# Kernel tuning notes

Hardware: AMD Instinct MI355X
Metric: run time of the kernel (lower is better)

The kernel has to match this reference:

```python
import jax, jax.numpy as jnp
import numpy as np

L_LEVELS = 16
N_FEATS = 2
BASE_RES = 16
LOG2_T = 19
T = 2 ** LOG2_T
BOUND = 1.0
DESIRED_RES = 2048 * BOUND
PER_LEVEL_SCALE = np.exp2(np.log2(DESIRED_RES / BASE_RES) / (L_LEVELS - 1))
PRIMES = np.array([1, 2654435761, 805459861], dtype=np.uint32)
# 8 trilinear corner offsets, [8,3]
OFFSETS = np.array([[(i >> d) & 1 for d in range(3)] for i in range(8)], dtype=np.uint32)


def hash_encode(x, table):
    """x: [N,3] in [-bound,bound]; table: [L, T, F]. Returns [N, L*F]."""
    x01 = jnp.clip((x + BOUND) / (2.0 * BOUND), 0.0, 1.0)  # [N,3]
    feats = []
    for l in range(L_LEVELS):
        scale = BASE_RES * (PER_LEVEL_SCALE ** l) - 1.0  # torch-ngp gridencoder convention
        res = int(np.ceil(scale)) + 1
        pos = x01 * jnp.float32(scale) + 0.5
        pg = jnp.floor(pos)
        frac = pos - pg                                   # [N,3]
        pgi = pg.astype(jnp.uint32)
        corners = pgi[:, None, :] + OFFSETS[None, :, :]   # [N,8,3] uint32
        if res ** 3 <= T:
            # grid small enough: direct (strided) indexing
            r = np.uint32(res)
            idx = corners[..., 0] + corners[..., 1] * r + corners[..., 2] * (r * r)
        else:
            # spatial hash (xor of coord*prime)
            idx = (corners[..., 0] * PRIMES[0]) ^ (corners[..., 1] * PRIMES[1]) ^ (corners[..., 2] * PRIMES[2])
        idx = (idx % np.uint32(T)).astype(jnp.int32)      # [N,8]
        f = table[l][idx]                                 # [N,8,F] gather
        # trilinear weights: prod over dims of frac (if corner bit=1) else 1-frac
        w = jnp.prod(jnp.where(OFFSETS[None, :, :] == 1, frac[:, None, :], 1.0 - frac[:, None, :]), axis=-1)  # [N,8]
        feats.append(jnp.sum(f * w[..., None], axis=1))   # [N,F]
    return jnp.concatenate(feats, axis=-1)                # [N, L*F]


def softplus_beta100(x):
    z = 100.0 * x
    return jnp.where(z > 20.0, x, jnp.log1p(jnp.exp(jnp.minimum(z, 20.0))) / 100.0)


def setup_inputs() -> dict:
    key = jax.random.key(0)
    k = jax.random.split(key, 6)
    N = 1048576
    in_dim = L_LEVELS * N_FEATS  # 32
    hidden = 64
    out_dim = 1 + 15             # sdf + geo_feat
    x = jax.random.uniform(k[0], (N, 3), jnp.float32, -1.0, 1.0)
    table = jax.random.uniform(k[1], (L_LEVELS, T, N_FEATS), jnp.float32, -1e-4, 1e-4)
    W0 = jax.random.normal(k[2], (hidden, in_dim), jnp.float32) * (1.0 / np.sqrt(in_dim))
    b0 = jnp.zeros((hidden,), jnp.float32)
    W1 = jax.random.normal(k[3], (out_dim, hidden), jnp.float32) * (1.0 / np.sqrt(hidden))
    b1 = jnp.zeros((out_dim,), jnp.float32)
    return {"x": x, "table": table, "W0": W0, "b0": b0, "W1": W1, "b1": b1}


def reference(x, table, W0, b0, W1, b1):
    enc = hash_encode(x, table)                      # [N,32]
    h = softplus_beta100(enc @ W0.T + b0)            # [N,64]
    h = h @ W1.T + b1                                # [N,16]
    sdf = h[..., :1]
    geo_feat = h[..., 1:]
    return (sdf, geo_feat)
```

## Files before the change

kernel.cpp:

```cpp
#include <hip/hip_runtime.h>
#include <math.h>

constexpr int      kLevels = 16;
constexpr unsigned kT      = 1u << 19;
constexpr int      kHidden = 64;
constexpr int      kInDim  = 32;
constexpr int      kOutDim = 16;

struct LevelParams {
    float    scale[kLevels];
    unsigned res[kLevels];
    unsigned dense[kLevels];
};

typedef __attribute__((ext_vector_type(8))) short bf16x8;
typedef __attribute__((ext_vector_type(4))) float f32x4;
typedef __attribute__((ext_vector_type(2))) unsigned uint2v;

__device__ inline float bf2f(unsigned short b) {
    unsigned u = ((unsigned)b) << 16;
    return __builtin_bit_cast(float, u);
}
__device__ inline unsigned short f2bf(float f) {
    unsigned u = __builtin_bit_cast(unsigned, f);
    unsigned r = (u + 0x7fffu + ((u >> 16) & 1u)) >> 16;
    return (unsigned short)r;
}
__device__ inline unsigned pack2bf(float a, float b) {
    return (unsigned)f2bf(a) | ((unsigned)f2bf(b) << 16);
}

__global__ __launch_bounds__(256) void convert_table(
        const float* __restrict__ t, unsigned* __restrict__ o, int n4)
{
    int i = blockIdx.x * blockDim.x + threadIdx.x;
    if (i >= n4) return;
    float4 v = ((const float4*)t)[i];
    ((uint2*)o)[i] = make_uint2(pack2bf(v.x, v.y), pack2bf(v.z, v.w));
}

__global__ __launch_bounds__(256) void encode_level(
        const float* __restrict__ x,
        const unsigned* __restrict__ tblAll,
        unsigned* __restrict__ enc,
        int N, LevelParams lp)
{
    const int l   = blockIdx.y;
    const int tid = threadIdx.x;
    const int pA  = blockIdx.x * 512 + tid;

    const float    scale = lp.scale[l];
    const unsigned res   = lp.res[l];
    const bool     dense = (lp.dense[l] != 0);
    const unsigned* tbl  = tblAll + (size_t)l * kT;

    #pragma unroll
    for (int half = 0; half < 2; ++half) {
        const int p = pA + half * 256;
        if (p >= N) continue;

        const float x0 = fminf(fmaxf((x[3 * p + 0] + 1.0f) * 0.5f, 0.0f), 1.0f);
        const float y0 = fminf(fmaxf((x[3 * p + 1] + 1.0f) * 0.5f, 0.0f), 1.0f);
        const float z0 = fminf(fmaxf((x[3 * p + 2] + 1.0f) * 0.5f, 0.0f), 1.0f);

        const float posx = x0 * scale + 0.5f;
        const float posy = y0 * scale + 0.5f;
        const float posz = z0 * scale + 0.5f;
        const float fgx = floorf(posx), fgy = floorf(posy), fgz = floorf(posz);
        const float fx = posx - fgx, fy = posy - fgy, fz = posz - fgz;
        const float gx = 1.0f - fx,  gy = 1.0f - fy,  gz = 1.0f - fz;
        const unsigned ix = (unsigned)fgx, iy = (unsigned)fgy, iz = (unsigned)fgz;

        unsigned v0[4], v1[4];
        float    wyz[4];

        #pragma unroll
        for (int c2 = 0; c2 < 4; ++c2) {
            const unsigned cy = iy + (c2 & 1);
            const unsigned cz = iz + (c2 >> 1);
            wyz[c2] = ((c2 & 1) ? fy : gy) * ((c2 >> 1) ? fz : gz);

            if (dense) {
                const unsigned base = cy * res + cz * res * res;
                const unsigned idx0 = (ix + base) & (kT - 1u);
                if ((idx0 & 1u) == 0u) {
                    const uint2v pr = *(const uint2v*)(tbl + idx0);
                    v0[c2] = pr.x; v1[c2] = pr.y;
                } else {
                    v0[c2] = tbl[idx0];
                    v1[c2] = tbl[idx0 + 1u];
                }
            } else {
                const unsigned base = (cy * 2654435761u) ^ (cz * 805459861u);
                const unsigned idx0 = (ix ^ base) & (kT - 1u);
                if ((ix & 1u) == 0u) {
                    const unsigned b = idx0 & ~1u;
                    const uint2v pr = *(const uint2v*)(tbl + b);
                    const bool sw = (idx0 & 1u) != 0u;
                    v0[c2] = sw ? pr.y : pr.x;
                    v1[c2] = sw ? pr.x : pr.y;
                } else {
                    const unsigned idx1 = ((ix + 1u) ^ base) & (kT - 1u);
                    v0[c2] = tbl[idx0];
                    v1[c2] = tbl[idx1];
                }
            }
        }

        float a0 = 0.0f, a1 = 0.0f;
        #pragma unroll
        for (int c2 = 0; c2 < 4; ++c2) {
            const float w0 = gx * wyz[c2];
            const float w1 = fx * wyz[c2];
            a0 = fmaf(bf2f((unsigned short)(v0[c2] & 0xffffu)), w0, a0);
            a1 = fmaf(bf2f((unsigned short)(v0[c2] >> 16)),     w0, a1);
            a0 = fmaf(bf2f((unsigned short)(v1[c2] & 0xffffu)), w1, a0);
            a1 = fmaf(bf2f((unsigned short)(v1[c2] >> 16)),     w1, a1);
        }
        enc[(size_t)l * N + p] = pack2bf(a0, a1);
    }
}

__global__ __launch_bounds__(256) void mlp_mfma(
        const unsigned* __restrict__ enc,
        const float* __restrict__ W0,
        const float* __restrict__ b0,
        const float* __restrict__ W1,
        const float* __restrict__ b1,
        float* __restrict__ out, int N, int nTiles)
{
    constexpr int kHStride = 72;
    __shared__ short lds_h[4][16 * kHStride];

    const int wave = threadIdx.x >> 6;
    const int lane = threadIdx.x & 63;
    const int quad = lane >> 4;
    const int l16  = lane & 15;

    union Frag { bf16x8 v; short s[8]; unsigned u[4]; };

    Frag w0f[4];
    #pragma unroll
    for (int hb = 0; hb < 4; ++hb) {
        #pragma unroll
        for (int j = 0; j < 8; ++j) {
            const int k = quad * 8 + j;
            const int n = hb * 16 + l16;
            w0f[hb].s[j] = (short)f2bf(W0[n * kInDim + k]);
        }
    }
    Frag w1f[2];
    #pragma unroll
    for (int kb = 0; kb < 2; ++kb) {
        #pragma unroll
        for (int j = 0; j < 8; ++j) {
            const int k = kb * 32 + quad * 8 + j;
            const int n = l16;
            w1f[kb].s[j] = (short)f2bf(W1[n * kHidden + k]);
        }
    }
    float b0v[4];
    #pragma unroll
    for (int hb = 0; hb < 4; ++hb) b0v[hb] = b0[hb * 16 + l16];
    const float b1v = b1[l16];

    short* hrow = lds_h[wave];
    const int waveGlobal = blockIdx.x * 4 + wave;
    const int nWaves     = gridDim.x * 4;

    for (int t = waveGlobal; t < nTiles; t += nWaves) {
        const int P = t * 16;
        int p = P + l16;
        if (p >= N) p = N - 1;

        Frag af;
        #pragma unroll
        for (int j2 = 0; j2 < 4; ++j2)
            af.u[j2] = enc[(size_t)(quad * 4 + j2) * N + p];

        f32x4 acc[4];
        #pragma unroll
        for (int hb = 0; hb < 4; ++hb) {
            acc[hb] = f32x4{b0v[hb], b0v[hb], b0v[hb], b0v[hb]};
            acc[hb] = __builtin_amdgcn_mfma_f32_16x16x32_bf16(
                          af.v, w0f[hb].v, acc[hb], 0, 0, 0);
        }

        #pragma unroll
        for (int hb = 0; hb < 4; ++hb) {
            #pragma unroll
            for (int r = 0; r < 4; ++r) {
                const float a = acc[hb][r];
                const float z = 100.0f * a;
                const float h = (z > 20.0f) ? a
                              : (__logf(1.0f + __expf(z)) * 0.01f);
                const int row = quad * 4 + r;
                const int col = hb * 16 + l16;
                hrow[row * kHStride + col] = (short)f2bf(h);
            }
        }
        bf16x8 h0 = *(const bf16x8*)&hrow[l16 * kHStride + quad * 8];
        bf16x8 h1 = *(const bf16x8*)&hrow[l16 * kHStride + 32 + quad * 8];

        f32x4 acc2 = f32x4{b1v, b1v, b1v, b1v};
        acc2 = __builtin_amdgcn_mfma_f32_16x16x32_bf16(h0, w1f[0].v, acc2, 0, 0, 0);
        acc2 = __builtin_amdgcn_mfma_f32_16x16x32_bf16(h1, w1f[1].v, acc2, 0, 0, 0);

        #pragma unroll
        for (int r = 0; r < 4; ++r) {
            const int pp = P + quad * 4 + r;
            if (pp < N) {
                if (l16 == 0) out[pp] = acc2[r];
                else out[(size_t)N + (size_t)pp * 15u + (l16 - 1)] = acc2[r];
            }
        }
    }
}

__global__ __launch_bounds__(256) void sdf_fused(
        const float* __restrict__ x, const float* __restrict__ table,
        const float* __restrict__ W0, const float* __restrict__ b0,
        const float* __restrict__ W1, const float* __restrict__ b1,
        float* __restrict__ out, int N, LevelParams lp)
{
    const int gid = blockIdx.x * blockDim.x + threadIdx.x;
    if (gid >= N) return;
    const float x0 = fminf(fmaxf((x[3 * gid + 0] + 1.0f) * 0.5f, 0.0f), 1.0f);
    const float y0 = fminf(fmaxf((x[3 * gid + 1] + 1.0f) * 0.5f, 0.0f), 1.0f);
    const float z0 = fminf(fmaxf((x[3 * gid + 2] + 1.0f) * 0.5f, 0.0f), 1.0f);
    float enc[kInDim];
    #pragma unroll
    for (int l = 0; l < kLevels; ++l) {
        const float scale = lp.scale[l];
        const unsigned res = lp.res[l];
        const bool dense = (lp.dense[l] != 0);
        const float posx = x0 * scale + 0.5f, posy = y0 * scale + 0.5f, posz = z0 * scale + 0.5f;
        const float fgx = floorf(posx), fgy = floorf(posy), fgz = floorf(posz);
        const float fx = posx - fgx, fy = posy - fgy, fz = posz - fgz;
        const float gx = 1.0f - fx, gy = 1.0f - fy, gz = 1.0f - fz;
        const unsigned ix = (unsigned)fgx, iy = (unsigned)fgy, iz = (unsigned)fgz;
        const float* tbl = table + (size_t)l * kT * 2u;
        float a0 = 0.0f, a1 = 0.0f;
        #pragma unroll
        for (int c = 0; c < 8; ++c) {
            const unsigned cx = ix + (c & 1), cy = iy + ((c >> 1) & 1), cz = iz + ((c >> 2) & 1);
            unsigned idx = dense ? (cx + cy * res + cz * res * res)
                                 : (cx ^ (cy * 2654435761u) ^ (cz * 805459861u));
            idx &= (kT - 1u);
            const float2 tv = *(const float2*)(tbl + 2u * idx);
            const float w = ((c & 1) ? fx : gx) * (((c >> 1) & 1) ? fy : gy) * (((c >> 2) & 1) ? fz : gz);
            a0 = fmaf(tv.x, w, a0); a1 = fmaf(tv.y, w, a1);
        }
        enc[2 * l] = a0; enc[2 * l + 1] = a1;
    }
    float acc[kOutDim];
    #pragma unroll
    for (int k = 0; k < kOutDim; ++k) acc[k] = b1[k];
    #pragma unroll 2
    for (int j = 0; j < kHidden; ++j) {
        float a = b0[j];
        #pragma unroll
        for (int i = 0; i < kInDim; ++i) a = fmaf(enc[i], W0[j * kInDim + i], a);
        const float z = 100.0f * a;
        const float h = (z > 20.0f) ? a : (__logf(1.0f + __expf(z)) * 0.01f);
        #pragma unroll
        for (int k = 0; k < kOutDim; ++k) acc[k] = fmaf(h, W1[k * kHidden + j], acc[k]);
    }
    out[gid] = acc[0];
    #pragma unroll
    for (int k = 0; k < 15; ++k) out[(size_t)N + (size_t)gid * 15u + k] = acc[k + 1];
}

extern "C" void kernel_launch(void* const* d_in, const int* in_sizes, int n_in,
                              void* d_out, int out_size, void* d_ws, size_t ws_size,
                              hipStream_t stream) {
    const float* x     = (const float*)d_in[0];
    const float* table = (const float*)d_in[1];
    const float* W0    = (const float*)d_in[2];
    const float* b0    = (const float*)d_in[3];
    const float* W1    = (const float*)d_in[4];
    const float* b1    = (const float*)d_in[5];
    float* out = (float*)d_out;
    const int N = in_sizes[0] / 3;

    LevelParams lp;
    const double s = exp2(7.0 / 15.0);
    for (int l = 0; l < kLevels; ++l) {
        const double sc = 16.0 * pow(s, (double)l) - 1.0;
        lp.scale[l] = (float)sc;
        const unsigned res = (unsigned)ceil(sc) + 1u;
        lp.res[l] = res;
        lp.dense[l] =
            ((unsigned long long)res * res * res <= (unsigned long long)kT) ? 1u : 0u;
    }

    const size_t tbl_bytes = (size_t)kLevels * kT * 4u;
    const size_t enc_bytes = (size_t)kLevels * (size_t)N * 4u;

    if (ws_size >= tbl_bytes + enc_bytes) {
        unsigned* tbl_bf = (unsigned*)d_ws;
        unsigned* enc    = (unsigned*)((char*)d_ws + tbl_bytes);

        const int n4 = (int)(kLevels * kT * 2u / 4u);
        hipLaunchKernelGGL(convert_table, dim3((n4 + 255) / 256), dim3(256), 0, stream,
                           table, tbl_bf, n4);

        dim3 gridA((N + 511) / 512, kLevels);
        hipLaunchKernelGGL(encode_level, gridA, dim3(256), 0, stream,
                           x, tbl_bf, enc, N, lp);

        const int nTiles = (N + 15) / 16;
        hipLaunchKernelGGL(mlp_mfma, dim3(2048), dim3(256), 0, stream,
                           enc, W0, b0, W1, b1, out, N, nTiles);
    } else {
        hipLaunchKernelGGL(sdf_fused, dim3((N + 255) / 256), dim3(256), 0, stream,
                           x, table, W0, b0, W1, b1, out, N, lp);
    }
}
```

Before: 449.0 us.

## Fuse hash encoding into MFMA MLP kernel, eliminating encoded intermediate buffer

The per-level encode kernel is merged into the MLP kernel. Each lane now computes the four levels it feeds into the MFMA A fragment directly from x and the bf16 table, so the 64 MB encoding buffer is never written to or read back from global memory. The cost is that all levels of a point are gathered inside one wave, which loses the per-level cache locality of the level-major grid. It also raises register pressure (16 pairs of gathered values per lane) and uses a fixed grid of 2048 blocks that may hide gather latency less well.

Measured after the change: 732.7 us. +63.2%, slower.

```diff
diff --git a/kernel.cpp b/kernel.cpp
--- a/kernel.cpp
+++ b/kernel.cpp
@@ -39,95 +39,14 @@
     ((uint2*)o)[i] = make_uint2(pack2bf(v.x, v.y), pack2bf(v.z, v.w));
 }
 
-__global__ __launch_bounds__(256) void encode_level(
+__global__ __launch_bounds__(256) void fused_enc_mlp(
         const float* __restrict__ x,
         const unsigned* __restrict__ tblAll,
-        unsigned* __restrict__ enc,
-        int N, LevelParams lp)
-{
-    const int l   = blockIdx.y;
-    const int tid = threadIdx.x;
-    const int pA  = blockIdx.x * 512 + tid;
-
-    const float    scale = lp.scale[l];
-    const unsigned res   = lp.res[l];
-    const bool     dense = (lp.dense[l] != 0);
-    const unsigned* tbl  = tblAll + (size_t)l * kT;
-
-    #pragma unroll
-    for (int half = 0; half < 2; ++half) {
-        const int p = pA + half * 256;
-        if (p >= N) continue;
-
-        const float x0 = fminf(fmaxf((x[3 * p + 0] + 1.0f) * 0.5f, 0.0f), 1.0f);
-        const float y0 = fminf(fmaxf((x[3 * p + 1] + 1.0f) * 0.5f, 0.0f), 1.0f);
-        const float z0 = fminf(fmaxf((x[3 * p + 2] + 1.0f) * 0.5f, 0.0f), 1.0f);
-
-        const float posx = x0 * scale + 0.5f;
-        const float posy = y0 * scale + 0.5f;
-        const float posz = z0 * scale + 0.5f;
-        const float fgx = floorf(posx), fgy = floorf(posy), fgz = floorf(posz);
-        const float fx = posx - fgx, fy = posy - fgy, fz = posz - fgz;
-        const float gx = 1.0f - fx,  gy = 1.0f - fy,  gz = 1.0f - fz;
-        const unsigned ix = (unsigned)fgx, iy = (unsigned)fgy, iz = (unsigned)fgz;
-
-        unsigned v0[4], v1[4];
-        float    wyz[4];
-
-        #pragma unroll
-        for (int c2 = 0; c2 < 4; ++c2) {
-            const unsigned cy = iy + (c2 & 1);
-            const unsigned cz = iz + (c2 >> 1);
-            wyz[c2] = ((c2 & 1) ? fy : gy) * ((c2 >> 1) ? fz : gz);
-
-            if (dense) {
-                const unsigned base = cy * res + cz * res * res;
-                const unsigned idx0 = (ix + base) & (kT - 1u);
-                if ((idx0 & 1u) == 0u) {
-                    const uint2v pr = *(const uint2v*)(tbl + idx0);
-                    v0[c2] = pr.x; v1[c2] = pr.y;
-                } else {
-                    v0[c2] = tbl[idx0];
-                    v1[c2] = tbl[idx0 + 1u];
-                }
-            } else {
-                const unsigned base = (cy * 2654435761u) ^ (cz * 805459861u);
-                const unsigned idx0 = (ix ^ base) & (kT - 1u);
-                if ((ix & 1u) == 0u) {
-                    const unsigned b = idx0 & ~1u;
-                    const uint2v pr = *(const uint2v*)(tbl + b);
-                    const bool sw = (idx0 & 1u) != 0u;
-                    v0[c2] = sw ? pr.y : pr.x;
-                    v1[c2] = sw ? pr.x : pr.y;
-                } else {
-                    const unsigned idx1 = ((ix + 1u) ^ base) & (kT - 1u);
-                    v0[c2] = tbl[idx0];
-                    v1[c2] = tbl[idx1];
-                }
-            }
-        }
-
-        float a0 = 0.0f, a1 = 0.0f;
-        #pragma unroll
-        for (int c2 = 0; c2 < 4; ++c2) {
-            const float w0 = gx * wyz[c2];
-            const float w1 = fx * wyz[c2];
-            a0 = fmaf(bf2f((unsigned short)(v0[c2] & 0xffffu)), w0, a0);
-            a1 = fmaf(bf2f((unsigned short)(v0[c2] >> 16)),     w0, a1);
-            a0 = fmaf(bf2f((unsigned short)(v1[c2] & 0xffffu)), w1, a0);
-            a1 = fmaf(bf2f((unsigned short)(v1[c2] >> 16)),     w1, a1);
-        }
-        enc[(size_t)l * N + p] = pack2bf(a0, a1);
-    }
-}
-
-__global__ __launch_bounds__(256) void mlp_mfma(
-        const unsigned* __restrict__ enc,
         const float* __restrict__ W0,
         const float* __restrict__ b0,
         const float* __restrict__ W1,
         const float* __restrict__ b1,
-        float* __restrict__ out, int N, int nTiles)
+        float* __restrict__ out, int N, int nTiles, LevelParams lp)
 {
     constexpr int kHStride = 72;
     __shared__ short lds_h[4][16 * kHStride];
@@ -164,6 +83,20 @@
     for (int hb = 0; hb < 4; ++hb) b0v[hb] = b0[hb * 16 + l16];
     const float b1v = b1[l16];
 
+    float    lscale[4];
+    unsigned lres[4];
+    unsigned ldense[4];
+    #pragma unroll
+    for (int j2 = 0; j2 < 4; ++j2) {
+        const int myl = quad * 4 + j2;
+        float sc = lp.scale[0]; unsigned rs = lp.res[0]; unsigned dn = lp.dense[0];
+        #pragma unroll
+        for (int ll = 1; ll < kLevels; ++ll) {
+            if (myl == ll) { sc = lp.scale[ll]; rs = lp.res[ll]; dn = lp.dense[ll]; }
+        }
+        lscale[j2] = sc; lres[j2] = rs; ldense[j2] = dn;
+    }
+
     short* hrow = lds_h[wave];
     const int waveGlobal = blockIdx.x * 4 + wave;
     const int nWaves     = gridDim.x * 4;
@@ -173,10 +106,79 @@
         int p = P + l16;
         if (p >= N) p = N - 1;
 
+        const float x0 = fminf(fmaxf((x[3 * p + 0] + 1.0f) * 0.5f, 0.0f), 1.0f);
+        const float y0 = fminf(fmaxf((x[3 * p + 1] + 1.0f) * 0.5f, 0.0f), 1.0f);
+        const float z0 = fminf(fmaxf((x[3 * p + 2] + 1.0f) * 0.5f, 0.0f), 1.0f);
+
+        unsigned v0[4][4], v1[4][4];
+        float    ffx[4], ffy[4], ffz[4];
+
+        #pragma unroll
+        for (int j2 = 0; j2 < 4; ++j2) {
+            const unsigned* tbl = tblAll + (size_t)(quad * 4 + j2) * kT;
+            const float scale = lscale[j2];
+            const unsigned res = lres[j2];
+            const bool dense = (ldense[j2] != 0);
+
+            const float posx = x0 * scale + 0.5f;
+            const float posy = y0 * scale + 0.5f;
+            const float posz = z0 * scale + 0.5f;
+            const float fgx = floorf(posx), fgy = floorf(posy), fgz = floorf(posz);
+            const float fx = posx - fgx, fy = posy - fgy, fz = posz - fgz;
+            const unsigned ix = (unsigned)fgx, iy = (unsigned)fgy, iz = (unsigned)fgz;
+            ffx[j2] = fx; ffy[j2] = fy; ffz[j2] = fz;
+
+            #pragma unroll
+            for (int c2 = 0; c2 < 4; ++c2) {
+                const unsigned cy = iy + (c2 & 1);
+                const unsigned cz = iz + (c2 >> 1);
+
+                if (dense) {
+                    const unsigned base = cy * res + cz * res * res;
+                    const unsigned idx0 = (ix + base) & (kT - 1u);
+                    if ((idx0 & 1u) == 0u) {
+                        const uint2v pr = *(const uint2v*)(tbl + idx0);
+                        v0[j2][c2] = pr.x; v1[j2][c2] = pr.y;
+                    } else {
+                        v0[j2][c2] = tbl[idx0];
+                        v1[j2][c2] = tbl[idx0 + 1u];
+                    }
+                } else {
+                    const unsigned base = (cy * 2654435761u) ^ (cz * 805459861u);
+                    const unsigned idx0 = (ix ^ base) & (kT - 1u);
+                    if ((ix & 1u) == 0u) {
+                        const unsigned b = idx0 & ~1u;
+                        const uint2v pr = *(const uint2v*)(tbl + b);
+                        const bool sw = (idx0 & 1u) != 0u;
+                        v0[j2][c2] = sw ? pr.y : pr.x;
+                        v1[j2][c2] = sw ? pr.x : pr.y;
+                    } else {
+                        const unsigned idx1 = ((ix + 1u) ^ base) & (kT - 1u);
+                        v0[j2][c2] = tbl[idx0];
+                        v1[j2][c2] = tbl[idx1];
+                    }
+                }
+            }
+        }
+
         Frag af;
         #pragma unroll
-        for (int j2 = 0; j2 < 4; ++j2)
-            af.u[j2] = enc[(size_t)(quad * 4 + j2) * N + p];
+        for (int j2 = 0; j2 < 4; ++j2) {
+            const float fx = ffx[j2], fy = ffy[j2], fz = ffz[j2];
+            const float gx = 1.0f - fx, gy = 1.0f - fy, gz = 1.0f - fz;
+            float a0 = 0.0f, a1 = 0.0f;
+            #pragma unroll
+            for (int c2 = 0; c2 < 4; ++c2) {
+                const float wyz = ((c2 & 1) ? fy : gy) * ((c2 >> 1) ? fz : gz);
+                const float w0 = gx * wyz;
+                const float w1 = fx * wyz;
+                a0 = fmaf(bf2f((unsigned short)(v0[j2][c2] & 0xffffu)), w0, a0);
+                a1 = fmaf(bf2f((unsigned short)(v0[j2][c2] >> 16)),     w0, a1);
+                a0 = fmaf(bf2f((unsigned short)(v1[j2][c2] & 0xffffu)), w1, a0);
+                a1 = fmaf(bf2f((unsigned short)(v1[j2][c2] >> 16)),     w1, a1);
+            }
+            af.u[j2] = pack2bf(a0, a1);
+        }
 
         f32x4 acc[4];
         #pragma unroll
@@ -295,23 +297,17 @@
     }
 
     const size_t tbl_bytes = (size_t)kLevels * kT * 4u;
-    const size_t enc_bytes = (size_t)kLevels * (size_t)N * 4u;
-
-    if (ws_size >= tbl_bytes + enc_bytes) {
+
+    if (ws_size >= tbl_bytes) {
         unsigned* tbl_bf = (unsigned*)d_ws;
-        unsigned* enc    = (unsigned*)((char*)d_ws + tbl_bytes);
 
         const int n4 = (int)(kLevels * kT * 2u / 4u);
         hipLaunchKernelGGL(convert_table, dim3((n4 + 255) / 256), dim3(256), 0, stream,
                            table, tbl_bf, n4);
 
-        dim3 gridA((N + 511) / 512, kLevels);
-        hipLaunchKernelGGL(encode_level, gridA, dim3(256), 0, stream,
-                           x, tbl_bf, enc, N, lp);
-
         const int nTiles = (N + 15) / 16;
-        hipLaunchKernelGGL(mlp_mfma, dim3(2048), dim3(256), 0, stream,
-                           enc, W0, b0, W1, b1, out, N, nTiles);
+        hipLaunchKernelGGL(fused_enc_mlp, dim3(2048), dim3(256), 0, stream,
+                           x, tbl_bf, W0, b0, W1, b1, out, N, nTiles, lp);
     } else {
         hipLaunchKernelGGL(sdf_fused, dim3((N + 255) / 256), dim3(256), 0, stream,
                            x, table, W0, b0, W1, b1, out, N, lp);
```

## Fuse hash-grid encoding and MFMA MLP into one persistent block kernel

Applied to the files above, without the earlier changes.

Replaces the separate per-level encode kernel and MLP kernel with a single persistent kernel. Each thread encodes all 16 levels for one point, stages the bf16 features in LDS, and the waves then run the MFMA MLP on 16-point tiles taken from LDS. This removes the global round trip of the encoded features and one launch. The cost is that level-major gather locality is lost: each thread now touches all 16 tables, rather than each block working on a single level's table as before, so L2 hit rates may drop. Register pressure also rises under the 256,4 launch bounds.

Measured after the change: 620.7 us. 1.38x slower.

```diff
diff --git a/kernel.cpp b/kernel.cpp
--- a/kernel.cpp
+++ b/kernel.cpp
@@ -16,6 +16,7 @@
 typedef __attribute__((ext_vector_type(8))) short bf16x8;
 typedef __attribute__((ext_vector_type(4))) float f32x4;
 typedef __attribute__((ext_vector_type(2))) unsigned uint2v;
+typedef __attribute__((ext_vector_type(4))) unsigned uint4v;
 
 __device__ inline float bf2f(unsigned short b) {
     unsigned u = ((unsigned)b) << 16;
@@ -39,101 +40,23 @@
     ((uint2*)o)[i] = make_uint2(pack2bf(v.x, v.y), pack2bf(v.z, v.w));
 }
 
-__global__ __launch_bounds__(256) void encode_level(
+__global__ __launch_bounds__(256, 4) void fused_block(
         const float* __restrict__ x,
         const unsigned* __restrict__ tblAll,
-        unsigned* __restrict__ enc,
-        int N, LevelParams lp)
-{
-    const int l   = blockIdx.y;
-    const int tid = threadIdx.x;
-    const int pA  = blockIdx.x * 512 + tid;
-
-    const float    scale = lp.scale[l];
-    const unsigned res   = lp.res[l];
-    const bool     dense = (lp.dense[l] != 0);
-    const unsigned* tbl  = tblAll + (size_t)l * kT;
-
-    #pragma unroll
-    for (int half = 0; half < 2; ++half) {
-        const int p = pA + half * 256;
-        if (p >= N) continue;
-
-        const float x0 = fminf(fmaxf((x[3 * p + 0] + 1.0f) * 0.5f, 0.0f), 1.0f);
-        const float y0 = fminf(fmaxf((x[3 * p + 1] + 1.0f) * 0.5f, 0.0f), 1.0f);
-        const float z0 = fminf(fmaxf((x[3 * p + 2] + 1.0f) * 0.5f, 0.0f), 1.0f);
-
-        const float posx = x0 * scale + 0.5f;
-        const float posy = y0 * scale + 0.5f;
-        const float posz = z0 * scale + 0.5f;
-        const float fgx = floorf(posx), fgy = floorf(posy), fgz = floorf(posz);
-        const float fx = posx - fgx, fy = posy - fgy, fz = posz - fgz;
-        const float gx = 1.0f - fx,  gy = 1.0f - fy,  gz = 1.0f - fz;
-        const unsigned ix = (unsigned)fgx, iy = (unsigned)fgy, iz = (unsigned)fgz;
-
-        unsigned v0[4], v1[4];
-        float    wyz[4];
-
-        #pragma unroll
-        for (int c2 = 0; c2 < 4; ++c2) {
-            const unsigned cy = iy + (c2 & 1);
-            const unsigned cz = iz + (c2 >> 1);
-            wyz[c2] = ((c2 & 1) ? fy : gy) * ((c2 >> 1) ? fz : gz);
-
-            if (dense) {
-                const unsigned base = cy * res + cz * res * res;
-                const unsigned idx0 = (ix + base) & (kT - 1u);
-                if ((idx0 & 1u) == 0u) {
-                    const uint2v pr = *(const uint2v*)(tbl + idx0);
-                    v0[c2] = pr.x; v1[c2] = pr.y;
-                } else {
-                    v0[c2] = tbl[idx0];
-                    v1[c2] = tbl[idx0 + 1u];
-                }
-            } else {
-                const unsigned base = (cy * 2654435761u) ^ (cz * 805459861u);
-                const unsigned idx0 = (ix ^ base) & (kT - 1u);
-                if ((ix & 1u) == 0u) {
-                    const unsigned b = idx0 & ~1u;
-                    const uint2v pr = *(const uint2v*)(tbl + b);
-                    const bool sw = (idx0 & 1u) != 0u;
-                    v0[c2] = sw ? pr.y : pr.x;
-                    v1[c2] = sw ? pr.x : pr.y;
-                } else {
-                    const unsigned idx1 = ((ix + 1u) ^ base) & (kT - 1u);
-                    v0[c2] = tbl[idx0];
-                    v1[c2] = tbl[idx1];
-                }
-            }
-        }
-
-        float a0 = 0.0f, a1 = 0.0f;
-        #pragma unroll
-        for (int c2 = 0; c2 < 4; ++c2) {
-            const float w0 = gx * wyz[c2];
-            const float w1 = fx * wyz[c2];
-            a0 = fmaf(bf2f((unsigned short)(v0[c2] & 0xffffu)), w0, a0);
-            a1 = fmaf(bf2f((unsigned short)(v0[c2] >> 16)),     w0, a1);
-            a0 = fmaf(bf2f((unsigned short)(v1[c2] & 0xffffu)), w1, a0);
-            a1 = fmaf(bf2f((unsigned short)(v1[c2] >> 16)),     w1, a1);
-        }
-        enc[(size_t)l * N + p] = pack2bf(a0, a1);
-    }
-}
-
-__global__ __launch_bounds__(256) void mlp_mfma(
-        const unsigned* __restrict__ enc,
         const float* __restrict__ W0,
         const float* __restrict__ b0,
         const float* __restrict__ W1,
         const float* __restrict__ b1,
-        float* __restrict__ out, int N, int nTiles)
+        float* __restrict__ out, int N, int nChunks, LevelParams lp)
 {
+    constexpr int kEncStride = 20;
     constexpr int kHStride = 72;
+    __shared__ unsigned enc_lds[256 * kEncStride];
     __shared__ short lds_h[4][16 * kHStride];
 
-    const int wave = threadIdx.x >> 6;
-    const int lane = threadIdx.x & 63;
+    const int tid  = threadIdx.x;
+    const int wave = tid >> 6;
+    const int lane = tid & 63;
     const int quad = lane >> 4;
     const int l16  = lane & 15;
 
@@ -165,55 +88,135 @@
     const float b1v = b1[l16];
 
     short* hrow = lds_h[wave];
-    const int waveGlobal = blockIdx.x * 4 + wave;
-    const int nWaves     = gridDim.x * 4;
-
-    for (int t = waveGlobal; t < nTiles; t += nWaves) {
-        const int P = t * 16;
-        int p = P + l16;
+
+    for (int chunk = blockIdx.x; chunk < nChunks; chunk += gridDim.x) {
+        const int base = chunk * 256;
+
+        int p = base + tid;
         if (p >= N) p = N - 1;
-
-        Frag af;
-        #pragma unroll
-        for (int j2 = 0; j2 < 4; ++j2)
-            af.u[j2] = enc[(size_t)(quad * 4 + j2) * N + p];
-
-        f32x4 acc[4];
-        #pragma unroll
-        for (int hb = 0; hb < 4; ++hb) {
-            acc[hb] = f32x4{b0v[hb], b0v[hb], b0v[hb], b0v[hb]};
-            acc[hb] = __builtin_amdgcn_mfma_f32_16x16x32_bf16(
-                          af.v, w0f[hb].v, acc[hb], 0, 0, 0);
-        }
-
-        #pragma unroll
-        for (int hb = 0; hb < 4; ++hb) {
+        const float x0 = fminf(fmaxf((x[3 * p + 0] + 1.0f) * 0.5f, 0.0f), 1.0f);
+        const float y0 = fminf(fmaxf((x[3 * p + 1] + 1.0f) * 0.5f, 0.0f), 1.0f);
+        const float z0 = fminf(fmaxf((x[3 * p + 2] + 1.0f) * 0.5f, 0.0f), 1.0f);
+
+        #pragma unroll
+        for (int lb = 0; lb < 4; ++lb) {
+            unsigned encq[4];
+            #pragma unroll
+            for (int j = 0; j < 4; ++j) {
+                const int l = lb * 4 + j;
+                const float    scale = lp.scale[l];
+                const unsigned res   = lp.res[l];
+                const bool     dense = (lp.dense[l] != 0);
+                const unsigned* tbl  = tblAll + (size_t)l * kT;
+
+                const float posx = x0 * scale + 0.5f;
+                const float posy = y0 * scale + 0.5f;
+                const float posz = z0 * scale + 0.5f;
+                const float fgx = floorf(posx), fgy = floorf(posy), fgz = floorf(posz);
+                const float fx = posx - fgx, fy = posy - fgy, fz = posz - fgz;
+                const float gx = 1.0f - fx,  gy = 1.0f - fy,  gz = 1.0f - fz;
+                const unsigned ix = (unsigned)fgx, iy = (unsigned)fgy, iz = (unsigned)fgz;
+
+                unsigned v0[4], v1[4];
+                float    wyz[4];
+                #pragma unroll
+                for (int c2 = 0; c2 < 4; ++c2) {
+                    const unsigned cy = iy + (c2 & 1);
+                    const unsigned cz = iz + (c2 >> 1);
+                    wyz[c2] = ((c2 & 1) ? fy : gy) * ((c2 >> 1) ? fz : gz);
+
+                    if (dense) {
+                        const unsigned bse = cy * res + cz * res * res;
+                        const unsigned idx0 = (ix + bse) & (kT - 1u);
+                        if ((idx0 & 1u) == 0u) {
+                            const uint2v pr = *(const uint2v*)(tbl + idx0);
+                            v0[c2] = pr.x; v1[c2] = pr.y;
+                        } else {
+                            v0[c2] = tbl[idx0];
+                            v1[c2] = tbl[idx0 + 1u];
+                        }
+                    } else {
+                        const unsigned bse = (cy * 2654435761u) ^ (cz * 805459861u);
+                        const unsigned idx0 = (ix ^ bse) & (kT - 1u);
+                        if ((ix & 1u) == 0u) {
+                            const unsigned b = idx0 & ~1u;
+                            const uint2v pr = *(const uint2v*)(tbl + b);
+                            const bool sw = (idx0 & 1u) != 0u;
+                            v0[c2] = sw ? pr.y : pr.x;
+                            v1[c2] = sw ? pr.x : pr.y;
+                        } else {
+                            const unsigned idx1 = ((ix + 1u) ^ bse) & (kT - 1u);
+                            v0[c2] = tbl[idx0];
+                            v1[c2] = tbl[idx1];
+                        }
+                    }
+                }
+
+                float a0 = 0.0f, a1 = 0.0f;
+                #pragma unroll
+                for (int c2 = 0; c2 < 4; ++c2) {
+                    const float w0w = gx * wyz[c2];
+                    const float w1w = fx * wyz[c2];
+                    a0 = fmaf(bf2f((unsigned short)(v0[c2] & 0xffffu)), w0w, a0);
+                    a1 = fmaf(bf2f((unsigned short)(v0[c2] >> 16)),     w0w, a1);
+                    a0 = fmaf(bf2f((unsigned short)(v1[c2] & 0xffffu)), w1w, a0);
+                    a1 = fmaf(bf2f((unsigned short)(v1[c2] >> 16)),     w1w, a1);
+                }
+                encq[j] = pack2bf(a0, a1);
+            }
+            *(uint4v*)&enc_lds[tid * kEncStride + lb * 4] =
+                uint4v{encq[0], encq[1], encq[2], encq[3]};
+        }
+
+        __syncthreads();
+
+        #pragma unroll
+        for (int tt = 0; tt < 4; ++tt) {
+            const int tileLocal = wave + tt * 4;
+            const int Plocal = tileLocal * 16;
+
+            Frag af;
+            af = *(const Frag*)&enc_lds[(Plocal + l16) * kEncStride + quad * 4];
+
+            f32x4 acc[4];
+            #pragma unroll
+            for (int hb = 0; hb < 4; ++hb) {
+                acc[hb] = f32x4{b0v[hb], b0v[hb], b0v[hb], b0v[hb]};
+                acc[hb] = __builtin_amdgcn_mfma_f32_16x16x32_bf16(
+                              af.v, w0f[hb].v, acc[hb], 0, 0, 0);
+            }
+
+            #pragma unroll
+            for (int hb = 0; hb < 4; ++hb) {
+                #pragma unroll
+                for (int r = 0; r < 4; ++r) {
+                    const float a = acc[hb][r];
+                    const float z = 100.0f * a;
+                    const float h = (z > 20.0f) ? a
+                                  : (__logf(1.0f + __expf(z)) * 0.01f);
+                    const int row = quad * 4 + r;
+                    const int col = hb * 16 + l16;
+                    hrow[row * kHStride + col] = (short)f2bf(h);
+                }
+            }
+            bf16x8 h0 = *(const bf16x8*)&hrow[l16 * kHStride + quad * 8];
+            bf16x8 h1 = *(const bf16x8*)&hrow[l16 * kHStride + 32 + quad * 8];
+
+            f32x4 acc2 = f32x4{b1v, b1v, b1v, b1v};
+            acc2 = __builtin_amdgcn_mfma_f32_16x16x32_bf16(h0, w1f[0].v, acc2, 0, 0, 0);
+            acc2 = __builtin_amdgcn_mfma_f32_16x16x32_bf16(h1, w1f[1].v, acc2, 0, 0, 0);
+
             #pragma unroll
             for (int r = 0; r < 4; ++r) {
-                const float a = acc[hb][r];
-                const float z = 100.0f * a;
-                const float h = (z > 20.0f) ? a
-                              : (__logf(1.0f + __expf(z)) * 0.01f);
-                const int row = quad * 4 + r;
-                const int col = hb * 16 + l16;
-                hrow[row * kHStride + col] = (short)f2bf(h);
+                const int pp = base + Plocal + quad * 4 + r;
+                if (pp < N) {
+                    if (l16 == 0) out[pp] = acc2[r];
+                    else out[(size_t)N + (size_t)pp * 15u + (l16 - 1)] = acc2[r];
+                }
             }
         }
-        bf16x8 h0 = *(const bf16x8*)&hrow[l16 * kHStride + quad * 8];
-        bf16x8 h1 = *(const bf16x8*)&hrow[l16 * kHStride + 32 + quad * 8];
-
-        f32x4 acc2 = f32x4{b1v, b1v, b1v, b1v};
-        acc2 = __builtin_amdgcn_mfma_f32_16x16x32_bf16(h0, w1f[0].v, acc2, 0, 0, 0);
-        acc2 = __builtin_amdgcn_mfma_f32_16x16x32_bf16(h1, w1f[1].v, acc2, 0, 0, 0);
-
-        #pragma unroll
-        for (int r = 0; r < 4; ++r) {
-            const int pp = P + quad * 4 + r;
-            if (pp < N) {
-                if (l16 == 0) out[pp] = acc2[r];
-                else out[(size_t)N + (size_t)pp * 15u + (l16 - 1)] = acc2[r];
-            }
-        }
+
+        __syncthreads();
     }
 }
 
@@ -295,23 +298,17 @@
     }
 
     const size_t tbl_bytes = (size_t)kLevels * kT * 4u;
-    const size_t enc_bytes = (size_t)kLevels * (size_t)N * 4u;
-
-    if (ws_size >= tbl_bytes + enc_bytes) {
+
+    if (ws_size >= tbl_bytes) {
         unsigned* tbl_bf = (unsigned*)d_ws;
-        unsigned* enc    = (unsigned*)((char*)d_ws + tbl_bytes);
 
         const int n4 = (int)(kLevels * kT * 2u / 4u);
         hipLaunchKernelGGL(convert_table, dim3((n4 + 255) / 256), dim3(256), 0, stream,
                            table, tbl_bf, n4);
 
-        dim3 gridA((N + 511) / 512, kLevels);
-        hipLaunchKernelGGL(encode_level, gridA, dim3(256), 0, stream,
-                           x, tbl_bf, enc, N, lp);
-
-        const int nTiles = (N + 15) / 16;
-        hipLaunchKernelGGL(mlp_mfma, dim3(2048), dim3(256), 0, stream,
-                           enc, W0, b0, W1, b1, out, N, nTiles);
+        const int nChunks = (N + 255) / 256;
+        hipLaunchKernelGGL(fused_block, dim3(1024), dim3(256), 0, stream,
+                           x, tbl_bf, W0, b0, W1, b1, out, N, nChunks, lp);
     } else {
         hipLaunchKernelGGL(sdf_fused, dim3((N + 255) / 256), dim3(256), 0, stream,
                            x, table, W0, b0, W1, b1, out, N, lp);
```
